# Kernel optimization log

Hardware: AMD Instinct MI355X
Metric: run time of the kernel (lower is better)

## Reference

```python
import jax, jax.numpy as jnp
import numpy as np

B, S, D = 2, 2048, 1024
H = 16
HD = D // H  # 64


def setup_inputs() -> dict:
    key = jax.random.key(0)
    ks = jax.random.split(key, 9)
    scale = 1.0 / np.sqrt(D)
    x = jax.random.normal(ks[0], (B, S, D), dtype=jnp.float32)
    Wq = jax.random.normal(ks[1], (D, D), dtype=jnp.float32) * scale
    bq = jnp.zeros((D,), dtype=jnp.float32)
    Wk = jax.random.normal(ks[2], (D, D), dtype=jnp.float32) * scale
    bk = jnp.zeros((D,), dtype=jnp.float32)
    Wv = jax.random.normal(ks[3], (D, D), dtype=jnp.float32) * scale
    bv = jnp.zeros((D,), dtype=jnp.float32)
    Wo = jax.random.normal(ks[4], (D, D), dtype=jnp.float32) * scale
    bo = jnp.zeros((D,), dtype=jnp.float32)
    return {"x": x, "Wq": Wq, "bq": bq, "Wk": Wk, "bk": bk,
            "Wv": Wv, "bv": bv, "Wo": Wo, "bo": bo}


def reference(x, Wq, bq, Wk, bk, Wv, bv, Wo, bo):
    b, s, d = x.shape
    # QKV projections (PhotonicCore == dim->dim linear)
    Q = x @ Wq + bq
    K = x @ Wk + bk
    V = x @ Wv + bv
    # [B, H, S, HD]
    Q = Q.reshape(b, s, H, HD).transpose(0, 2, 1, 3)
    K = K.reshape(b, s, H, HD).transpose(0, 2, 1, 3)
    V = V.reshape(b, s, H, HD).transpose(0, 2, 1, 3)
    # full [B, H, S, S] scores, exactly as the original (unfused) module
    scores = jnp.einsum("bhqd,bhkd->bhqk", Q, K) / jnp.sqrt(jnp.asarray(HD, x.dtype))
    weights = jax.nn.softmax(scores, axis=-1)
    attn = jnp.einsum("bhqk,bhkd->bhqd", weights, V)
    attn = attn.transpose(0, 2, 1, 3).reshape(b, s, d)
    return attn @ Wo + bo
```

## Files before the change

kernel.cpp:

```cpp
#include <hip/hip_runtime.h>
#include <stdint.h>

typedef unsigned short u16;
typedef unsigned int u32;
typedef unsigned long long u64;
typedef __bf16 bf16x8 __attribute__((ext_vector_type(8)));
typedef float f32x4 __attribute__((ext_vector_type(4)));
typedef unsigned short u16x8 __attribute__((ext_vector_type(8)));
typedef unsigned short u16x4 __attribute__((ext_vector_type(4)));

#define QSCALE 0.1803368801111204f

static __device__ __forceinline__ u16 f2bf(float f) {
  unsigned u = __builtin_bit_cast(unsigned, f);
  u += 0x7fffu + ((u >> 16) & 1u);
  return (u16)(u >> 16);
}

static __device__ __forceinline__ bf16x8 ldfrag(const u16* p) {
  return *reinterpret_cast<const bf16x8*>(p);
}

static __device__ __forceinline__ void gll16(const u16* g, u16* l) {
  __builtin_amdgcn_global_load_lds(
      (const __attribute__((address_space(1))) void*)g,
      (__attribute__((address_space(3))) void*)l, 16, 0, 0);
}

static __device__ __forceinline__ u32 cvt_pk_bf16(float lo, float hi) {
  u32 r;
  asm("v_cvt_pk_bf16_f32 %0, %1, %2" : "=v"(r) : "v"(lo), "v"(hi));
  return r;
}

static __device__ __forceinline__ float fexp2(float x) {
  return __builtin_amdgcn_exp2f(x);
}

static __device__ __forceinline__ float fm3(float a, float b, float c) {
  return fmaxf(fmaxf(a, b), c);
}

__global__ __launch_bounds__(256) void cast_x_kernel(const float* __restrict__ x,
                                                     u16* __restrict__ xb) {
  int i = (blockIdx.x * 256 + threadIdx.x) * 8;
  const float4* p = reinterpret_cast<const float4*>(x + i);
  float4 a = p[0], b = p[1];
  u16x8 o;
  o[0] = f2bf(a.x); o[1] = f2bf(a.y); o[2] = f2bf(a.z); o[3] = f2bf(a.w);
  o[4] = f2bf(b.x); o[5] = f2bf(b.y); o[6] = f2bf(b.z); o[7] = f2bf(b.w);
  *reinterpret_cast<u16x8*>(xb + i) = o;
}

__global__ __launch_bounds__(256) void transpose_w_kernel(
    const float* __restrict__ Wq, const float* __restrict__ Wk,
    const float* __restrict__ Wv, const float* __restrict__ Wo,
    u16* __restrict__ WT) {
  __shared__ float tile[64][65];
  int z = blockIdx.z;
  const float* W = (z == 0) ? Wq : (z == 1) ? Wk : (z == 2) ? Wv : Wo;
  float wscale = (z == 0) ? QSCALE : 1.0f;
  u16* out = WT + (size_t)z * 1024 * 1024;
  int k0 = blockIdx.y * 64, n0 = blockIdx.x * 64;
  int t = threadIdx.x;
  int rr = t >> 4;
  int cc = (t & 15) * 4;
#pragma unroll
  for (int j = 0; j < 4; ++j) {
    int r = rr + 16 * j;
    float4 v = *reinterpret_cast<const float4*>(W + (size_t)(k0 + r) * 1024 + n0 + cc);
    tile[r][cc + 0] = v.x; tile[r][cc + 1] = v.y;
    tile[r][cc + 2] = v.z; tile[r][cc + 3] = v.w;
  }
  __syncthreads();
#pragma unroll
  for (int j = 0; j < 4; ++j) {
    int nl = rr + 16 * j;
    u16x4 o;
#pragma unroll
    for (int i2 = 0; i2 < 4; ++i2) o[i2] = f2bf(tile[cc + i2][nl] * wscale);
    *reinterpret_cast<u16x4*>(out + (size_t)(n0 + nl) * 1024 + k0 + cc) = o;
  }
}

template <int MODE>
static __device__ __forceinline__ void qkv_body(
    u16* smem, const u16* __restrict__ A, const u16* __restrict__ Wt,
    const float* __restrict__ bias, float bscale, u16* __restrict__ Out) {
  u16* As = smem;
  u16* Bs = smem + 4096;
  int t = threadIdx.x;
  int lane = t & 63, wave = t >> 6;
  int g = lane >> 4, c = lane & 15;
  int m0 = blockIdx.y * 128, n0 = blockIdx.x * 128;
  int wm = (wave >> 1) * 32, wn = (wave & 1) * 64;

  f32x4 acc[2][4] = {};

  const u16* Ag = A + (size_t)(m0 + (t >> 2)) * 1024 + (t & 3) * 8;
  const u16* Bg = Wt + (size_t)(n0 + (t >> 2)) * 1024 + (t & 3) * 8;
  u16* Asd = As + t * 8;
  u16* Bsd = Bs + t * 8;

  for (int k0 = 0; k0 < 1024; k0 += 32) {
    gll16(Ag + k0, Asd);
    gll16(Bg + k0, Bsd);
    __syncthreads();
    bf16x8 af[2], bfr[4];
#pragma unroll
    for (int i = 0; i < 2; ++i) af[i] = ldfrag(As + (wm + 16 * i + c) * 32 + g * 8);
#pragma unroll
    for (int j = 0; j < 4; ++j) bfr[j] = ldfrag(Bs + (wn + 16 * j + c) * 32 + g * 8);
#pragma unroll
    for (int i = 0; i < 2; ++i)
#pragma unroll
      for (int j = 0; j < 4; ++j) {
        if (MODE == 2)
          acc[i][j] = __builtin_amdgcn_mfma_f32_16x16x32_bf16(af[i], bfr[j], acc[i][j], 0, 0, 0);
        else
          acc[i][j] = __builtin_amdgcn_mfma_f32_16x16x32_bf16(bfr[j], af[i], acc[i][j], 0, 0, 0);
      }
    __syncthreads();
  }

  if (MODE == 0) {
    int nj[4], hj[4], dj[4];
    f32x4 bbj[4];
#pragma unroll
    for (int j = 0; j < 4; ++j) {
      nj[j] = n0 + wn + 16 * j + 4 * g;
      hj[j] = nj[j] >> 6; dj[j] = nj[j] & 63;
      f32x4 bb = *reinterpret_cast<const f32x4*>(&bias[nj[j]]);
#pragma unroll
      for (int r = 0; r < 4; ++r) bbj[j][r] = bb[r] * bscale;
    }
#pragma unroll
    for (int i = 0; i < 2; ++i) {
      int m = m0 + wm + 16 * i + c;
      int b2 = m >> 11, s2 = m & 2047;
#pragma unroll
      for (int j = 0; j < 4; ++j) {
        u16x4 o4;
#pragma unroll
        for (int r = 0; r < 4; ++r) o4[r] = f2bf(acc[i][j][r] + bbj[j][r]);
        *reinterpret_cast<u16x4*>(
            Out + ((size_t)(b2 * 16 + hj[j]) * 2048 + s2) * 64 + dj[j]) = o4;
      }
    }
  } else {
    float bvj[4];
#pragma unroll
    for (int j = 0; j < 4; ++j) bvj[j] = bias[n0 + wn + 16 * j + c];
    u16* tb = smem;
    int b2 = m0 >> 11, s0 = m0 & 2047;
    int rdrow = t >> 3;
    int slot = t & 7;
    int sh_base = ((wave >> 1) & 1) * 32;
#pragma unroll
    for (int half = 0; half < 2; ++half) {
      if ((wave >> 2) == half) {
#pragma unroll
        for (int i = 0; i < 2; ++i)
#pragma unroll
          for (int j = 0; j < 4; ++j) {
            u16x4 o4;
#pragma unroll
            for (int r = 0; r < 4; ++r) o4[r] = f2bf(acc[i][j][r] + bvj[j]);
            *reinterpret_cast<u16x4*>(
                &tb[(wn + 16 * j + c) * 72 + sh_base + 16 * i + 4 * g]) = o4;
          }
      }
      __syncthreads();
#pragma unroll
      for (int k = 0; k < 2; ++k) {
        int row = rdrow + 64 * k;
        u16x8 v = *reinterpret_cast<const u16x8*>(&tb[row * 72 + slot * 8]);
        int n = n0 + row, h2 = n >> 6, d2 = n & 63;
        *reinterpret_cast<u16x8*>(
            Out + ((size_t)(b2 * 16 + h2) * 64 + d2) * 2048 + s0 + half * 64 + slot * 8) = v;
      }
      if (half == 0) __syncthreads();
    }
  }
}

__global__ __launch_bounds__(512) void qkv_gemm_kernel(
    const u16* __restrict__ xb, const u16* __restrict__ WT,
    const float* __restrict__ bq, const float* __restrict__ bk,
    const float* __restrict__ bv,
    u16* __restrict__ Q, u16* __restrict__ K, u16* __restrict__ V) {
  __shared__ u16 smem[9216];
  int z = blockIdx.z;
  if (z == 0)      qkv_body<0>(smem, xb, WT, bq, QSCALE, Q);
  else if (z == 1) qkv_body<0>(smem, xb, WT + (size_t)1024 * 1024, bk, 1.0f, K);
  else             qkv_body<2>(smem, xb, WT + (size_t)2 * 1024 * 1024, bv, 1.0f, V);
}

__global__ __launch_bounds__(512) void oproj_kernel(
    const u16* __restrict__ A, const u16* __restrict__ Wt,
    const float* __restrict__ bias, float* __restrict__ out) {
  __shared__ u16 As[128 * 32];
  __shared__ u16 Bs[128 * 32];
  int t = threadIdx.x;
  int lane = t & 63, wave = t >> 6;
  int g = lane >> 4, c = lane & 15;
  int m0 = blockIdx.y * 128, n0 = blockIdx.x * 128;
  int wm = (wave >> 1) * 32, wn = (wave & 1) * 64;

  f32x4 acc[2][4] = {};

  const u16* Ag = A + (size_t)(m0 + (t >> 2)) * 1024 + (t & 3) * 8;
  const u16* Bg = Wt + (size_t)(n0 + (t >> 2)) * 1024 + (t & 3) * 8;
  u16* Asd = As + t * 8;
  u16* Bsd = Bs + t * 8;

  for (int k0 = 0; k0 < 1024; k0 += 32) {
    gll16(Ag + k0, Asd);
    gll16(Bg + k0, Bsd);
    __syncthreads();
    bf16x8 af[2], bfr[4];
#pragma unroll
    for (int i = 0; i < 2; ++i) af[i] = ldfrag(As + (wm + 16 * i + c) * 32 + g * 8);
#pragma unroll
    for (int j = 0; j < 4; ++j) bfr[j] = ldfrag(Bs + (wn + 16 * j + c) * 32 + g * 8);
#pragma unroll
    for (int i = 0; i < 2; ++i)
#pragma unroll
      for (int j = 0; j < 4; ++j)
        acc[i][j] = __builtin_amdgcn_mfma_f32_16x16x32_bf16(bfr[j], af[i], acc[i][j], 0, 0, 0);
    __syncthreads();
  }

  f32x4 bbj[4];
#pragma unroll
  for (int j = 0; j < 4; ++j)
    bbj[j] = *reinterpret_cast<const f32x4*>(&bias[n0 + wn + 16 * j + 4 * g]);
#pragma unroll
  for (int i = 0; i < 2; ++i) {
    int m = m0 + wm + 16 * i + c;
#pragma unroll
    for (int j = 0; j < 4; ++j) {
      f32x4 v = acc[i][j] + bbj[j];
      *reinterpret_cast<f32x4*>(out + (size_t)m * 1024 + n0 + wn + 16 * j + 4 * g) = v;
    }
  }
}

__global__ __launch_bounds__(512) void attn_kernel(
    const u16* __restrict__ Q, const u16* __restrict__ K,
    const u16* __restrict__ V, u16* __restrict__ attn) {
  __shared__ u16 Kf[3][4096];
  __shared__ u16 Vt[3][4096];
  __shared__ u16 Pf[8][512];

  const int t = threadIdx.x;
  const int lane = t & 63, w = t >> 6;
  const int g = lane >> 4, c = lane & 15;

  int flat = blockIdx.x + 16 * (blockIdx.y + 16 * blockIdx.z);
  int sw = (flat & 7) * 64 + (flat >> 3);
  const int b = sw >> 8, h = (sw >> 4) & 15, q0 = (sw & 15) * 128;

  const u16* Qh = Q + ((size_t)(b * 16 + h) * 2048) * 64;
  const u16* Kh = K + ((size_t)(b * 16 + h) * 2048) * 64;
  const u16* VTh = V + ((size_t)(b * 16 + h) * 64) * 2048;

  const int qw = q0 + w * 16;
  bf16x8 qf0 = ldfrag(Qh + (size_t)(qw + c) * 64 + 8 * g);
  bf16x8 qf1 = ldfrag(Qh + (size_t)(qw + c) * 64 + 32 + 8 * g);

  bf16x8 ones;
  {
    u16x8 tmp;
#pragma unroll
    for (int l = 0; l < 8; ++l) tmp[l] = 0x3F80;
    ones = __builtin_bit_cast(bf16x8, tmp);
  }

  const u16* ksrc = Kh + (size_t)(16 * ((w >> 1) & 3) + c) * 64 + 32 * (w & 1) + 8 * g;
  const u16* vsrc = VTh + (size_t)(8 * w + (lane >> 3)) * 2048 +
                    (((lane & 7) ^ ((lane >> 3) & 7)) * 8);

  const int koff = g * 128 + c * 8;
  int vb_off[2];
#pragma unroll
  for (int m = 0; m < 2; ++m)
    vb_off[m] = c * 64 + (((4 * m + g) ^ (c & 7)) * 8);
  const int pa_off = (g * 16 + c) * 8;

  f32x4 o[4] = {};
  f32x4 lsum = {};
  float mrow = -3e38f;

  gll16(ksrc, &Kf[0][t * 8]);
  gll16(vsrc, &Vt[0][t * 8]);
  gll16(ksrc + 4096, &Kf[1][t * 8]);
  gll16(vsrc + 64, &Vt[1][t * 8]);
  asm volatile("s_waitcnt vmcnt(2)" ::: "memory");
  __builtin_amdgcn_s_barrier();
  asm volatile("" ::: "memory");

  int cur = 0;
  for (int tt32 = 0; tt32 < 32; ++tt32) {
    if (tt32 <= 29) {
      int nb = cur + 2; if (nb >= 3) nb -= 3;
      gll16(ksrc + (size_t)(tt32 + 2) * 4096, &Kf[nb][t * 8]);
      gll16(vsrc + (size_t)(tt32 + 2) * 64, &Vt[nb][t * 8]);
    }

    const u16* kb = &Kf[cur][koff];
    f32x4 st[4];
    __builtin_amdgcn_s_setprio(1);
#pragma unroll
    for (int t4 = 0; t4 < 4; ++t4) {
      f32x4 acc = {};
      acc = __builtin_amdgcn_mfma_f32_16x16x32_bf16(
          ldfrag(kb + t4 * 1024), qf0, acc, 0, 0, 0);
      st[t4] = __builtin_amdgcn_mfma_f32_16x16x32_bf16(
          ldfrag(kb + t4 * 1024 + 512), qf1, acc, 0, 0, 0);
    }
    __builtin_amdgcn_s_setprio(0);

    float u1 = fm3(fm3(st[0][0], st[0][1], st[0][2]),
                   fm3(st[0][3], st[1][0], st[1][1]),
                   fm3(st[1][2], st[1][3], st[2][0]));
    float u2 = fm3(fm3(st[2][1], st[2][2], st[2][3]),
                   fm3(st[3][0], st[3][1], st[3][2]), st[3][3]);
    float tm = fmaxf(u1, u2);
    tm = fmaxf(tm, __shfl_xor(tm, 16));
    tm = fmaxf(tm, __shfl_xor(tm, 32));
    const bool grow = __any(tm > mrow + 8.0f);
    if (grow) {
      float nm = fmaxf(mrow, tm);
      float f = fexp2(mrow - nm);
      mrow = nm;
#pragma unroll
      for (int r = 0; r < 4; ++r) {
        float fr = __shfl(f, 4 * g + r);
        lsum[r] *= fr;
#pragma unroll
        for (int j = 0; j < 4; ++j) o[j][r] *= fr;
      }
    }
#pragma unroll
    for (int t4 = 0; t4 < 4; ++t4)
#pragma unroll
      for (int r = 0; r < 4; ++r) st[t4][r] = fexp2(st[t4][r] - mrow);

    u32* pd = (u32*)&Pf[w][0];
#pragma unroll
    for (int m = 0; m < 2; ++m) {
#pragma unroll
      for (int tp = 0; tp < 2; ++tp) {
        int t4 = 2 * m + tp;
        u32 w0 = cvt_pk_bf16(st[t4][0], st[t4][1]);
        u32 w1 = cvt_pk_bf16(st[t4][2], st[t4][3]);
        int gp = (2 * t4 + (g >> 1)) & 3;
        int base = (gp * 16 + c) * 4 + 2 * (g & 1);
        *reinterpret_cast<u64*>(&pd[base]) = (u64)w0 | ((u64)w1 << 32);
      }
      bf16x8 pa = ldfrag(&Pf[w][pa_off]);
      __builtin_amdgcn_s_setprio(1);
#pragma unroll
      for (int j = 0; j < 4; ++j) {
        bf16x8 vb = ldfrag(&Vt[cur][vb_off[m] + j * 1024]);
        o[j] = __builtin_amdgcn_mfma_f32_16x16x32_bf16(pa, vb, o[j], 0, 0, 0);
      }
      lsum = __builtin_amdgcn_mfma_f32_16x16x32_bf16(pa, ones, lsum, 0, 0, 0);
      __builtin_amdgcn_s_setprio(0);
    }

    if (tt32 <= 29)
      asm volatile("s_waitcnt vmcnt(2)" ::: "memory");
    else if (tt32 == 30)
      asm volatile("s_waitcnt vmcnt(0)" ::: "memory");
    if (tt32 < 31) {
      __builtin_amdgcn_s_barrier();
      asm volatile("" ::: "memory");
    }
    ++cur; if (cur == 3) cur = 0;
  }

  float rinv[4];
#pragma unroll
  for (int r = 0; r < 4; ++r) rinv[r] = 1.f / lsum[r];
#pragma unroll
  for (int j = 0; j < 4; ++j)
#pragma unroll
    for (int r = 0; r < 4; ++r) {
      int s = qw + 4 * g + r;
      attn[(size_t)(b * 2048 + s) * 1024 + h * 64 + 16 * j + c] = f2bf(o[j][r] * rinv[r]);
    }
}

extern "C" void kernel_launch(void* const* d_in, const int* in_sizes, int n_in,
                              void* d_out, int out_size, void* d_ws, size_t ws_size,
                              hipStream_t stream) {
  const float* x  = (const float*)d_in[0];
  const float* Wq = (const float*)d_in[1];
  const float* bq = (const float*)d_in[2];
  const float* Wk = (const float*)d_in[3];
  const float* bk = (const float*)d_in[4];
  const float* Wv = (const float*)d_in[5];
  const float* bv = (const float*)d_in[6];
  const float* Wo = (const float*)d_in[7];
  const float* bo = (const float*)d_in[8];
  float* out = (float*)d_out;
  u16* ws = (u16*)d_ws;

  u16* xb    = ws;
  u16* WT    = ws + (size_t)4 * 1024 * 1024;
  u16* Qb    = ws + (size_t)8 * 1024 * 1024;
  u16* Kb    = ws + (size_t)12 * 1024 * 1024;
  u16* Vb    = ws + (size_t)16 * 1024 * 1024;
  u16* attnb = xb;

  cast_x_kernel<<<2048, 256, 0, stream>>>(x, xb);
  transpose_w_kernel<<<dim3(16, 16, 4), 256, 0, stream>>>(Wq, Wk, Wv, Wo, WT);
  qkv_gemm_kernel<<<dim3(8, 32, 3), 512, 0, stream>>>(xb, WT, bq, bk, bv, Qb, Kb, Vb);
  attn_kernel<<<dim3(16, 16, 2), 512, 0, stream>>>(Qb, Kb, Vb, attnb);
  oproj_kernel<<<dim3(8, 32), 512, 0, stream>>>(attnb, WT + (size_t)3 * 1024 * 1024, bo, out);
}
```

Before: 138.0 us.

## Triple-buffer LDS loads in QKV and output projection GEMMs

Replaces the single-buffered load/sync/compute loop in the QKV and output projection GEMMs with a three-stage ring of LDS buffers. Tiles are prefetched two k-steps ahead via global_load_lds, with explicit vmcnt waits and one barrier per step instead of two. The MFMA block also gets raised wave priority. This trades more LDS per block (48KB) and possible occupancy loss for hiding global-memory latency behind compute.

Result: faster. 124.3 us (-9.9%).

```diff
diff --git a/kernel.cpp b/kernel.cpp
--- a/kernel.cpp
+++ b/kernel.cpp
@@ -87,8 +87,6 @@
 static __device__ __forceinline__ void qkv_body(
     u16* smem, const u16* __restrict__ A, const u16* __restrict__ Wt,
     const float* __restrict__ bias, float bscale, u16* __restrict__ Out) {
-  u16* As = smem;
-  u16* Bs = smem + 4096;
   int t = threadIdx.x;
   int lane = t & 63, wave = t >> 6;
   int g = lane >> 4, c = lane & 15;
@@ -99,18 +97,34 @@
 
   const u16* Ag = A + (size_t)(m0 + (t >> 2)) * 1024 + (t & 3) * 8;
   const u16* Bg = Wt + (size_t)(n0 + (t >> 2)) * 1024 + (t & 3) * 8;
-  u16* Asd = As + t * 8;
-  u16* Bsd = Bs + t * 8;
-
-  for (int k0 = 0; k0 < 1024; k0 += 32) {
-    gll16(Ag + k0, Asd);
-    gll16(Bg + k0, Bsd);
-    __syncthreads();
+
+  u16* dstA = smem + t * 8;
+  u16* dstB = smem + 4096 + t * 8;
+  const int afo = (wm + c) * 32 + g * 8;
+  const int bfo = 4096 + (wn + c) * 32 + g * 8;
+
+  gll16(Ag, dstA);
+  gll16(Bg, dstB);
+  gll16(Ag + 32, dstA + 8192);
+  gll16(Bg + 32, dstB + 8192);
+  asm volatile("s_waitcnt vmcnt(2)" ::: "memory");
+  __builtin_amdgcn_s_barrier();
+  asm volatile("" ::: "memory");
+
+  int cur = 0;
+  for (int st = 0; st < 32; ++st) {
+    if (st <= 29) {
+      int nb = cur + 2; if (nb >= 3) nb -= 3;
+      gll16(Ag + (st + 2) * 32, dstA + nb * 8192);
+      gll16(Bg + (st + 2) * 32, dstB + nb * 8192);
+    }
+    const u16* buf = smem + cur * 8192;
     bf16x8 af[2], bfr[4];
 #pragma unroll
-    for (int i = 0; i < 2; ++i) af[i] = ldfrag(As + (wm + 16 * i + c) * 32 + g * 8);
-#pragma unroll
-    for (int j = 0; j < 4; ++j) bfr[j] = ldfrag(Bs + (wn + 16 * j + c) * 32 + g * 8);
+    for (int i = 0; i < 2; ++i) af[i] = ldfrag(buf + afo + 16 * i * 32);
+#pragma unroll
+    for (int j = 0; j < 4; ++j) bfr[j] = ldfrag(buf + bfo + 16 * j * 32);
+    __builtin_amdgcn_s_setprio(1);
 #pragma unroll
     for (int i = 0; i < 2; ++i)
 #pragma unroll
@@ -120,7 +134,17 @@
         else
           acc[i][j] = __builtin_amdgcn_mfma_f32_16x16x32_bf16(bfr[j], af[i], acc[i][j], 0, 0, 0);
       }
-    __syncthreads();
+    __builtin_amdgcn_s_setprio(0);
+
+    if (st <= 29)
+      asm volatile("s_waitcnt vmcnt(2)" ::: "memory");
+    else if (st == 30)
+      asm volatile("s_waitcnt vmcnt(0)" ::: "memory");
+    if (st < 31) {
+      __builtin_amdgcn_s_barrier();
+      asm volatile("" ::: "memory");
+    }
+    ++cur; if (cur == 3) cur = 0;
   }
 
   if (MODE == 0) {
@@ -156,6 +180,7 @@
     int rdrow = t >> 3;
     int slot = t & 7;
     int sh_base = ((wave >> 1) & 1) * 32;
+    __syncthreads();
 #pragma unroll
     for (int half = 0; half < 2; ++half) {
       if ((wave >> 2) == half) {
@@ -189,7 +214,7 @@
     const float* __restrict__ bq, const float* __restrict__ bk,
     const float* __restrict__ bv,
     u16* __restrict__ Q, u16* __restrict__ K, u16* __restrict__ V) {
-  __shared__ u16 smem[9216];
+  __shared__ u16 smem[24576];
   int z = blockIdx.z;
   if (z == 0)      qkv_body<0>(smem, xb, WT, bq, QSCALE, Q);
   else if (z == 1) qkv_body<0>(smem, xb, WT + (size_t)1024 * 1024, bk, 1.0f, K);
@@ -199,8 +224,7 @@
 __global__ __launch_bounds__(512) void oproj_kernel(
     const u16* __restrict__ A, const u16* __restrict__ Wt,
     const float* __restrict__ bias, float* __restrict__ out) {
-  __shared__ u16 As[128 * 32];
-  __shared__ u16 Bs[128 * 32];
+  __shared__ u16 smem[24576];
   int t = threadIdx.x;
   int lane = t & 63, wave = t >> 6;
   int g = lane >> 4, c = lane & 15;
@@ -211,24 +235,49 @@
 
   const u16* Ag = A + (size_t)(m0 + (t >> 2)) * 1024 + (t & 3) * 8;
   const u16* Bg = Wt + (size_t)(n0 + (t >> 2)) * 1024 + (t & 3) * 8;
-  u16* Asd = As + t * 8;
-  u16* Bsd = Bs + t * 8;
-
-  for (int k0 = 0; k0 < 1024; k0 += 32) {
-    gll16(Ag + k0, Asd);
-    gll16(Bg + k0, Bsd);
-    __syncthreads();
+  u16* dstA = smem + t * 8;
+  u16* dstB = smem + 4096 + t * 8;
+  const int afo = (wm + c) * 32 + g * 8;
+  const int bfo = 4096 + (wn + c) * 32 + g * 8;
+
+  gll16(Ag, dstA);
+  gll16(Bg, dstB);
+  gll16(Ag + 32, dstA + 8192);
+  gll16(Bg + 32, dstB + 8192);
+  asm volatile("s_waitcnt vmcnt(2)" ::: "memory");
+  __builtin_amdgcn_s_barrier();
+  asm volatile("" ::: "memory");
+
+  int cur = 0;
+  for (int st = 0; st < 32; ++st) {
+    if (st <= 29) {
+      int nb = cur + 2; if (nb >= 3) nb -= 3;
+      gll16(Ag + (st + 2) * 32, dstA + nb * 8192);
+      gll16(Bg + (st + 2) * 32, dstB + nb * 8192);
+    }
+    const u16* buf = smem + cur * 8192;
     bf16x8 af[2], bfr[4];
 #pragma unroll
-    for (int i = 0; i < 2; ++i) af[i] = ldfrag(As + (wm + 16 * i + c) * 32 + g * 8);
-#pragma unroll
-    for (int j = 0; j < 4; ++j) bfr[j] = ldfrag(Bs + (wn + 16 * j + c) * 32 + g * 8);
+    for (int i = 0; i < 2; ++i) af[i] = ldfrag(buf + afo + 16 * i * 32);
+#pragma unroll
+    for (int j = 0; j < 4; ++j) bfr[j] = ldfrag(buf + bfo + 16 * j * 32);
+    __builtin_amdgcn_s_setprio(1);
 #pragma unroll
     for (int i = 0; i < 2; ++i)
 #pragma unroll
       for (int j = 0; j < 4; ++j)
         acc[i][j] = __builtin_amdgcn_mfma_f32_16x16x32_bf16(bfr[j], af[i], acc[i][j], 0, 0, 0);
-    __syncthreads();
+    __builtin_amdgcn_s_setprio(0);
+
+    if (st <= 29)
+      asm volatile("s_waitcnt vmcnt(2)" ::: "memory");
+    else if (st == 30)
+      asm volatile("s_waitcnt vmcnt(0)" ::: "memory");
+    if (st < 31) {
+      __builtin_amdgcn_s_barrier();
+      asm volatile("" ::: "memory");
+    }
+    ++cur; if (cur == 3) cur = 0;
   }
 
   f32x4 bbj[4];
```
